# Optimization experiments

Measured on AMD Instinct MI355X. Metric: run time of the kernel, lower is better.

## Reference

```python
import jax, jax.numpy as jnp
import numpy as np

DIM_HEAD = 64
HEADS = 8

def rotate_half(x):
    x1, x2 = jnp.split(x, 2, axis=-1)
    return jnp.concatenate((-x2, x1), axis=-1)

def apply_rope(pos, t):
    # pos: [N, d] broadcast against t: [B, H, N, d]
    return t * jnp.cos(pos) + rotate_half(t) * jnp.sin(pos)

def setup_inputs() -> dict:
    key = jax.random.key(0)
    k1, k2, k3, k4 = jax.random.split(key, 4)
    B, N, C = 2, 4096, 512
    inner = HEADS * DIM_HEAD
    x = jax.random.normal(k1, (B, N, C), dtype=jnp.float32)
    pos_emb = jax.random.normal(k2, (N, DIM_HEAD), dtype=jnp.float32)
    w_qkv = jax.random.normal(k3, (C, inner * 3), dtype=jnp.float32) * (1.0 / np.sqrt(C))
    w_out = jax.random.normal(k4, (inner, C), dtype=jnp.float32) * (1.0 / np.sqrt(inner))
    b_out = jnp.zeros((C,), dtype=jnp.float32)
    return {"x": x, "pos_emb": pos_emb, "w_qkv": w_qkv, "w_out": w_out, "b_out": b_out}

def reference(x, pos_emb, w_qkv, w_out, b_out):
    B, N, C = x.shape
    scale = DIM_HEAD ** -0.5
    qkv = x @ w_qkv  # [B, N, 3*inner]
    q, k, v = jnp.split(qkv, 3, axis=-1)
    def to_heads(t):
        return t.reshape(B, N, HEADS, DIM_HEAD).transpose(0, 2, 1, 3)  # [B,H,N,d]
    q, k, v = to_heads(q), to_heads(k), to_heads(v)
    q = apply_rope(pos_emb, q)
    k = apply_rope(pos_emb, k)
    dots = jnp.einsum('bhid,bhjd->bhij', q, k) * scale  # [B,H,N,N]
    attn = jax.nn.softmax(dots, axis=-1)
    out = jnp.einsum('bhij,bhjd->bhid', attn, v)
    out = out.transpose(0, 2, 1, 3).reshape(B, N, HEADS * DIM_HEAD)
    return out @ w_out + b_out
```

## Files before the change

### kernel.cpp

```cpp
#include <hip/hip_runtime.h>


typedef float    floatx4 __attribute__((ext_vector_type(4)));
typedef _Float16 half8   __attribute__((ext_vector_type(8)));
typedef _Float16 half4   __attribute__((ext_vector_type(4)));

__device__ __forceinline__ float fast_exp2(float x) {
#if __has_builtin(__builtin_amdgcn_exp2f)
  return __builtin_amdgcn_exp2f(x);
#else
  float r;
  asm("v_exp_f32 %0, %1" : "=v"(r) : "v"(x));
  return r;
#endif
}

__device__ __forceinline__ void async16(const void* g, void* l) {
  __builtin_amdgcn_global_load_lds(
      (const __attribute__((address_space(1))) void*)g,
      (__attribute__((address_space(3))) void*)l, 16, 0, 0);
}

__global__ __launch_bounds__(256) void prep(
    const float* __restrict__ X, const float* __restrict__ pos,
    const float* __restrict__ Wqkv, const float* __restrict__ Wout,
    _Float16* __restrict__ A2, float2* __restrict__ CSSN,
    _Float16* __restrict__ B2qkv, _Float16* __restrict__ B2out) {
  __shared__ float tile[64][65];
  const int bid = blockIdx.x, t = threadIdx.x;
  if (bid < 4096) {
    const int i = (bid * 256 + t) * 4;
    const float4 v = *(const float4*)(X + i);
    half4 h;
    h[0] = (_Float16)v.x; h[1] = (_Float16)v.y;
    h[2] = (_Float16)v.z; h[3] = (_Float16)v.w;
    *(half4*)(A2 + i) = h;
  } else if (bid < 5120) {
    const int i = (bid - 4096) * 256 + t;
    const float p = pos[i];
    CSSN[i] = make_float2(__cosf(p), __sinf(p));
  } else {
    const float* W; _Float16* B2T; int Ncols, bx, by;
    if (bid < 5312) { const int idx = bid - 5120; bx = idx % 24; by = idx / 24;
                      W = Wqkv; B2T = B2qkv; Ncols = 1536; }
    else            { const int idx = bid - 5312; bx = idx % 8;  by = idx / 8;
                      W = Wout; B2T = B2out; Ncols = 512; }
    const int k0 = by * 64, n0 = bx * 64;
    const int lane = t & 63, w = t >> 6;
#pragma unroll 4
    for (int i = 0; i < 16; ++i) {
      const int k = w * 16 + i;
      tile[k][lane] = W[(size_t)(k0 + k) * Ncols + n0 + lane];
    }
    __syncthreads();
#pragma unroll 4
    for (int i = 0; i < 16; ++i) {
      const int n = w * 16 + i;
      B2T[(size_t)(n0 + n) * 512 + k0 + lane] = (_Float16)tile[lane][n];
    }
  }
}

__global__ __launch_bounds__(256) void gemm_qkv_rope(
    const _Float16* __restrict__ A2, const _Float16* __restrict__ B2T,
    const float2* __restrict__ CSSN,
    _Float16* __restrict__ Qb, _Float16* __restrict__ Kb,
    _Float16* __restrict__ VT) {
  __shared__ __align__(16) _Float16 ldsA[128 * 64];
  __shared__ __align__(16) _Float16 ldsB[128 * 64];
  const int t = threadIdx.x, w = t >> 6, l = t & 63;
  const int lo = l & 15, hi = l >> 4, sw = lo & 7;
  const int m0 = blockIdx.y << 7, n0 = blockIdx.x << 7;

  const int strow = w * 8 + (l >> 3);
  const int schunk = (l & 7) ^ ((l >> 3) & 7);
  const _Float16* gA = A2 + (size_t)(m0 + strow) * 512 + schunk * 8;
  const _Float16* gB = B2T + (size_t)(n0 + strow) * 512 + schunk * 8;
  _Float16* lA = ldsA + w * 512 + l * 8;
  _Float16* lB = ldsB + w * 512 + l * 8;

  const int mw = (w >> 1) * 64, nw = (w & 1) * 64;

  floatx4 acc[4][4];
#pragma unroll
  for (int mt = 0; mt < 4; ++mt)
#pragma unroll
    for (int nt = 0; nt < 4; ++nt) acc[mt][nt] = (floatx4){0.f, 0.f, 0.f, 0.f};

  for (int ks = 0; ks < 8; ++ks) {
    const int kk = ks * 64;
    __syncthreads();
#pragma unroll
    for (int i = 0; i < 4; ++i) {
      async16(gA + (size_t)i * 32 * 512 + kk, lA + i * 2048);
      async16(gB + (size_t)i * 32 * 512 + kk, lB + i * 2048);
    }
    __syncthreads();
#pragma unroll
    for (int kc = 0; kc < 2; ++kc) {
      const int slot = ((hi + 4 * kc) ^ sw) * 8;
      half8 af[4], bf[4];
#pragma unroll
      for (int mt = 0; mt < 4; ++mt)
        af[mt] = *(const half8*)(ldsA + (mw + mt * 16 + lo) * 64 + slot);
#pragma unroll
      for (int nt = 0; nt < 4; ++nt)
        bf[nt] = *(const half8*)(ldsB + (nw + nt * 16 + lo) * 64 + slot);
#pragma unroll
      for (int mt = 0; mt < 4; ++mt)
#pragma unroll
        for (int nt = 0; nt < 4; ++nt)
          acc[mt][nt] = __builtin_amdgcn_mfma_f32_16x16x32_f16(
              af[mt], bf[nt], acc[mt][nt], 0, 0, 0);
    }
  }

  const int bx = blockIdx.x;
  const int kind = bx >> 2;
  const int h = ((bx & 3) << 1) | (nw >> 6);
  if (kind == 2) {
#pragma unroll
    for (int mt = 0; mt < 4; ++mt) {
      const int rowb = m0 + mw + mt * 16 + hi * 4;
      const int b = rowb >> 12, nn = rowb & 4095;
#pragma unroll
      for (int nt = 0; nt < 4; ++nt) {
        const int dd = nt * 16 + lo;
        half4 v4;
#pragma unroll
        for (int r = 0; r < 4; ++r) v4[r] = (_Float16)acc[mt][nt][r];
        *(half4*)(VT + ((size_t)((b * 8 + h) * 64 + dd)) * 4096 + nn) = v4;
      }
    }
  } else {
    _Float16* Db = (kind == 0) ? Qb : Kb;
    const float sc = (kind == 0) ? 0.125f * 1.44269504f : 1.0f;
#pragma unroll
    for (int mt = 0; mt < 4; ++mt)
#pragma unroll
      for (int r = 0; r < 4; ++r) {
        const int row = m0 + mw + mt * 16 + hi * 4 + r;
        const int b = row >> 12, nn = row & 4095;
        const float2* cp = CSSN + (size_t)nn * 64 + lo;
        _Float16* orow = Db + ((size_t)((b * 8 + h) * 4096 + nn)) * 64 + lo;
#pragma unroll
        for (int nt = 0; nt < 4; ++nt) {
          const float2 cs = cp[nt * 16];
          const float x0 = acc[mt][nt][r];
          const float xp = acc[mt][nt ^ 2][r];
          const float rot = (nt & 2) ? xp : -xp;
          orow[nt * 16] = (_Float16)((x0 * cs.x + rot * cs.y) * sc);
        }
      }
  }
}

__global__ __launch_bounds__(256) void gemm_out_f16(
    const _Float16* __restrict__ A2, const _Float16* __restrict__ B2T,
    const float* __restrict__ bias, float* __restrict__ C) {
  __shared__ __align__(16) _Float16 ldsA[128 * 64];
  __shared__ __align__(16) _Float16 ldsB[64 * 64];
  const int t = threadIdx.x, w = t >> 6, l = t & 63;
  const int lo = l & 15, hi = l >> 4, sw = lo & 7;
  const int m0 = blockIdx.y << 7, n0 = blockIdx.x << 6;

  const int strow = w * 8 + (l >> 3);
  const int schunk = (l & 7) ^ ((l >> 3) & 7);
  const _Float16* gA = A2 + (size_t)(m0 + strow) * 512 + schunk * 8;
  const _Float16* gB = B2T + (size_t)(n0 + strow) * 512 + schunk * 8;
  _Float16* lA = ldsA + w * 512 + l * 8;
  _Float16* lB = ldsB + w * 512 + l * 8;

  const int mw = (w >> 1) * 64, nw = (w & 1) * 32;

  floatx4 acc[4][2];
#pragma unroll
  for (int mt = 0; mt < 4; ++mt)
#pragma unroll
    for (int nt = 0; nt < 2; ++nt) acc[mt][nt] = (floatx4){0.f, 0.f, 0.f, 0.f};

  for (int ks = 0; ks < 8; ++ks) {
    const int kk = ks * 64;
    __syncthreads();
#pragma unroll
    for (int i = 0; i < 4; ++i)
      async16(gA + (size_t)i * 32 * 512 + kk, lA + i * 2048);
#pragma unroll
    for (int i = 0; i < 2; ++i)
      async16(gB + (size_t)i * 32 * 512 + kk, lB + i * 2048);
    __syncthreads();
#pragma unroll
    for (int kc = 0; kc < 2; ++kc) {
      const int slot = ((hi + 4 * kc) ^ sw) * 8;
      half8 af[4], bf[2];
#pragma unroll
      for (int mt = 0; mt < 4; ++mt)
        af[mt] = *(const half8*)(ldsA + (mw + mt * 16 + lo) * 64 + slot);
#pragma unroll
      for (int nt = 0; nt < 2; ++nt)
        bf[nt] = *(const half8*)(ldsB + (nw + nt * 16 + lo) * 64 + slot);
#pragma unroll
      for (int mt = 0; mt < 4; ++mt)
#pragma unroll
        for (int nt = 0; nt < 2; ++nt)
          acc[mt][nt] = __builtin_amdgcn_mfma_f32_16x16x32_f16(
              af[mt], bf[nt], acc[mt][nt], 0, 0, 0);
    }
  }
#pragma unroll
  for (int mt = 0; mt < 4; ++mt)
#pragma unroll
    for (int r = 0; r < 4; ++r) {
      const int row = m0 + mw + mt * 16 + hi * 4 + r;
#pragma unroll
      for (int nt = 0; nt < 2; ++nt) {
        const int col = n0 + nw + nt * 16 + lo;
        C[(size_t)row * 512 + col] = acc[mt][nt][r] + bias[col];
      }
    }
}

__global__ __launch_bounds__(256, 4) void flash_attn(
    const _Float16* __restrict__ Qb, const _Float16* __restrict__ Kb,
    const _Float16* __restrict__ VT, _Float16* __restrict__ Opart,
    float* __restrict__ lpart) {
  __shared__ __align__(16) _Float16 ldsK[64 * 64];
  __shared__ __align__(16) _Float16 ldsV[64 * 64];
  const int t = threadIdx.x;
  const int w = t >> 6, l = t & 63;
  const int lo = l & 15, hi = l >> 4;
  const int sw = lo & 7;
  const int bh = blockIdx.y, qt = blockIdx.x, sp = blockIdx.z;

  const int srow = l >> 3;
  const int scol = (l & 7) ^ srow;
  const int goffK = srow * 64 + scol * 8;
  const size_t goffV = (size_t)srow * 4096 + scol * 8;
  const int ldst = l * 8;

  const _Float16* Qrow = Qb + ((size_t)bh * 4096 + qt * 128 + w * 32 + lo) * 64;
  half8 qf[2][2];
  qf[0][0] = *(const half8*)(Qrow + hi * 8);
  qf[0][1] = *(const half8*)(Qrow + hi * 8 + 32);
  qf[1][0] = *(const half8*)(Qrow + 16 * 64 + hi * 8);
  qf[1][1] = *(const half8*)(Qrow + 16 * 64 + hi * 8 + 32);

  const half4 onesf = (lo == 0) ? (half4){1.f16, 1.f16, 1.f16, 1.f16}
                                : (half4){0.f16, 0.f16, 0.f16, 0.f16};

  floatx4 acc[2][4];
  floatx4 l_acc[2];
#pragma unroll
  for (int g = 0; g < 2; ++g) {
    l_acc[g] = (floatx4){0.f, 0.f, 0.f, 0.f};
#pragma unroll
    for (int dt = 0; dt < 4; ++dt) acc[g][dt] = (floatx4){0.f, 0.f, 0.f, 0.f};
  }

  const _Float16* Kt = Kb + (size_t)bh * 4096 * 64;
  const _Float16* Vt = VT + (size_t)bh * 64 * 4096;

  for (int tt = sp * 32; tt < sp * 32 + 32; ++tt) {
    __syncthreads();
    {
      const _Float16* gK = Kt + (size_t)tt * 4096;
      const _Float16* gV = Vt + tt * 64;
      const int k0 = w * 2;
      async16(gK + (size_t)k0 * 512 + goffK,       ldsK + k0 * 512 + ldst);
      async16(gK + (size_t)(k0 + 1) * 512 + goffK, ldsK + (k0 + 1) * 512 + ldst);
      async16(gV + (size_t)k0 * 32768 + goffV,       ldsV + k0 * 512 + ldst);
      async16(gV + (size_t)(k0 + 1) * 32768 + goffV, ldsV + (k0 + 1) * 512 + ldst);
    }
    __syncthreads();

    floatx4 st[2][4];
#pragma unroll
    for (int jt = 0; jt < 4; ++jt) {
      const _Float16* kr = ldsK + (jt * 16 + lo) * 64;
      const half8 kf0 = *(const half8*)(kr + ((hi ^ sw) * 8));
      const half8 kf1 = *(const half8*)(kr + (((hi + 4) ^ sw) * 8));
#pragma unroll
      for (int g = 0; g < 2; ++g) {
        floatx4 z = (floatx4){0.f, 0.f, 0.f, 0.f};
        z = __builtin_amdgcn_mfma_f32_16x16x32_f16(kf0, qf[g][0], z, 0, 0, 0);
        z = __builtin_amdgcn_mfma_f32_16x16x32_f16(kf1, qf[g][1], z, 0, 0, 0);
        st[g][jt] = z;
      }
    }

    half4 pf[2][4];
#pragma unroll
    for (int g = 0; g < 2; ++g)
#pragma unroll
      for (int jt = 0; jt < 4; ++jt) {
        const float e0 = fast_exp2(st[g][jt][0]);
        const float e1 = fast_exp2(st[g][jt][1]);
        const float e2 = fast_exp2(st[g][jt][2]);
        const float e3 = fast_exp2(st[g][jt][3]);
        uint2 u;
        u.x = __builtin_bit_cast(unsigned, __builtin_amdgcn_cvt_pkrtz(e0, e1));
        u.y = __builtin_bit_cast(unsigned, __builtin_amdgcn_cvt_pkrtz(e2, e3));
        const half4 p4 = __builtin_bit_cast(half4, u);
        pf[g][jt] = p4;
        l_acc[g] = __builtin_amdgcn_mfma_f32_16x16x16f16(
            p4, onesf, l_acc[g], 0, 0, 0);
      }

#pragma unroll
    for (int dt = 0; dt < 4; ++dt) {
      half4 vf[4];
#pragma unroll
      for (int jt = 0; jt < 4; ++jt)
        vf[jt] = *(const half4*)(ldsV + (dt * 16 + lo) * 64 +
                                 (((jt * 2 + (hi >> 1)) ^ sw) * 8) + (hi & 1) * 4);
#pragma unroll
      for (int g = 0; g < 2; ++g)
#pragma unroll
        for (int jt = 0; jt < 4; ++jt)
          acc[g][dt] = __builtin_amdgcn_mfma_f32_16x16x16f16(
              pf[g][jt], vf[jt], acc[g][dt], 0, 0, 0);
    }
  }

  _Float16* obase = Opart + ((size_t)(sp * 16 + bh)) * 4096 * 64;
  float*    lbase = lpart + ((size_t)(sp * 16 + bh)) * 4096;
#pragma unroll
  for (int g = 0; g < 2; ++g)
#pragma unroll
    for (int r = 0; r < 4; ++r) {
      const int q = qt * 128 + w * 32 + g * 16 + hi * 4 + r;
      if (lo == 0) lbase[q] = l_acc[g][r];
#pragma unroll
      for (int dt = 0; dt < 4; ++dt)
        obase[(size_t)q * 64 + dt * 16 + lo] = (_Float16)acc[g][dt][r];
    }
}

__global__ __launch_bounds__(256) void combine_splits(
    const _Float16* __restrict__ Opart, const float* __restrict__ lpart,
    _Float16* __restrict__ O2) {
  const int idx = blockIdx.x * 256 + threadIdx.x;
  const int d0 = (idx & 15) * 4;
  const int q  = (idx >> 4) & 4095;
  const int bh = idx >> 16;
  const int b = bh >> 3, h = bh & 7;
  const half4 a0 = *(const half4*)(Opart + ((size_t)bh * 4096 + q) * 64 + d0);
  const half4 a1 = *(const half4*)(Opart + ((size_t)(16 + bh) * 4096 + q) * 64 + d0);
  const float lsum = lpart[(size_t)bh * 4096 + q] +
                     lpart[(size_t)(16 + bh) * 4096 + q];
  const float inv = 1.f / lsum;
  half4 o;
#pragma unroll
  for (int i = 0; i < 4; ++i)
    o[i] = (_Float16)(((float)a0[i] + (float)a1[i]) * inv);
  *(half4*)(O2 + ((size_t)(b * 4096 + q)) * 512 + h * 64 + d0) = o;
}

extern "C" void kernel_launch(void* const* d_in, const int* in_sizes, int n_in,
                              void* d_out, int out_size, void* d_ws, size_t ws_size,
                              hipStream_t stream) {
  const float* x     = (const float*)d_in[0];
  const float* pos   = (const float*)d_in[1];
  const float* w_qkv = (const float*)d_in[2];
  const float* w_out = (const float*)d_in[3];
  const float* b_out = (const float*)d_in[4];
  float* out = (float*)d_out;

  char* ws = (char*)d_ws;
  if (ws_size < (size_t)56 * 1024 * 1024) return;

  const size_t MB = 1024 * 1024;
  _Float16* A2x   = (_Float16*)ws;
  _Float16* O2    = (_Float16*)ws;
  _Float16* B2qkv = (_Float16*)(ws + 8 * MB);
  float2*   CSSN  = (float2*)(ws + 11 * MB);
  _Float16* Qb    = (_Float16*)(ws + 13 * MB);
  _Float16* Kb    = (_Float16*)(ws + 21 * MB);
  _Float16* VT    = (_Float16*)(ws + 29 * MB);
  _Float16* Opart = (_Float16*)(ws + 37 * MB);
  float*    lpart = (float*)(ws + 53 * MB);
  _Float16* B2out = (_Float16*)(ws + 54 * MB);

  prep<<<5376, 256, 0, stream>>>(x, pos, w_qkv, w_out, A2x, CSSN, B2qkv, B2out);
  gemm_qkv_rope<<<dim3(12, 64), 256, 0, stream>>>(A2x, B2qkv, CSSN, Qb, Kb, VT);
  flash_attn<<<dim3(32, 16, 2), 256, 0, stream>>>(Qb, Kb, VT, Opart, lpart);
  combine_splits<<<4096, 256, 0, stream>>>(Opart, lpart, O2);
  gemm_out_f16<<<dim3(8, 64), 256, 0, stream>>>(O2, B2out, b_out, out);
}
```

Baseline: 211.0 us.

## Stage RoPE Q/K output through LDS and replace row-sum MFMA with VALU shuffles

The QKV GEMM epilogue now writes rotated Q/K values into a per-wave padded LDS tile, then stores whole 16-byte rows to global memory, replacing scattered 2-byte stores. In attention, the softmax denominator is no longer accumulated with an extra MFMA against a ones vector. It is summed per lane in fp32 and reduced across lane groups with xor shuffles at the end. This removes 8 MFMAs per tile iteration and improves store coalescing, at the cost of extra LDS traffic and VALU adds; the row sum now uses unrounded fp32 exponentials rather than the fp16-rounded ones.

```diff
diff --git a/kernel.cpp b/kernel.cpp
--- a/kernel.cpp
+++ b/kernel.cpp
@@ -68,6 +68,7 @@
     _Float16* __restrict__ VT) {
   __shared__ __align__(16) _Float16 ldsA[128 * 64];
   __shared__ __align__(16) _Float16 ldsB[128 * 64];
+  __shared__ __align__(16) _Float16 qk_lds[4][16][72];
   const int t = threadIdx.x, w = t >> 6, l = t & 63;
   const int lo = l & 15, hi = l >> 4, sw = lo & 7;
   const int m0 = blockIdx.y << 7, n0 = blockIdx.x << 7;
@@ -135,23 +136,33 @@
   } else {
     _Float16* Db = (kind == 0) ? Qb : Kb;
     const float sc = (kind == 0) ? 0.125f * 1.44269504f : 1.0f;
-#pragma unroll
-    for (int mt = 0; mt < 4; ++mt)
+    _Float16 (*qt_)[72] = qk_lds[w];
+#pragma unroll
+    for (int mt = 0; mt < 4; ++mt) {
 #pragma unroll
       for (int r = 0; r < 4; ++r) {
         const int row = m0 + mw + mt * 16 + hi * 4 + r;
-        const int b = row >> 12, nn = row & 4095;
+        const int nn = row & 4095;
         const float2* cp = CSSN + (size_t)nn * 64 + lo;
-        _Float16* orow = Db + ((size_t)((b * 8 + h) * 4096 + nn)) * 64 + lo;
 #pragma unroll
         for (int nt = 0; nt < 4; ++nt) {
           const float2 cs = cp[nt * 16];
           const float x0 = acc[mt][nt][r];
           const float xp = acc[mt][nt ^ 2][r];
           const float rot = (nt & 2) ? xp : -xp;
-          orow[nt * 16] = (_Float16)((x0 * cs.x + rot * cs.y) * sc);
+          qt_[hi * 4 + r][nt * 16 + lo] = (_Float16)((x0 * cs.x + rot * cs.y) * sc);
         }
       }
+#pragma unroll
+      for (int pass = 0; pass < 2; ++pass) {
+        const int rr = pass * 8 + (l >> 3);
+        const int dcol = (l & 7) * 8;
+        const half8 v = *(const half8*)&qt_[rr][dcol];
+        const int row = m0 + mw + mt * 16 + rr;
+        const int b = row >> 12, nn = row & 4095;
+        *(half8*)(Db + ((size_t)((b * 8 + h) * 4096 + nn)) * 64 + dcol) = v;
+      }
+    }
   }
 }
 
@@ -245,17 +256,12 @@
   qf[1][0] = *(const half8*)(Qrow + 16 * 64 + hi * 8);
   qf[1][1] = *(const half8*)(Qrow + 16 * 64 + hi * 8 + 32);
 
-  const half4 onesf = (lo == 0) ? (half4){1.f16, 1.f16, 1.f16, 1.f16}
-                                : (half4){0.f16, 0.f16, 0.f16, 0.f16};
-
   floatx4 acc[2][4];
-  floatx4 l_acc[2];
-#pragma unroll
-  for (int g = 0; g < 2; ++g) {
-    l_acc[g] = (floatx4){0.f, 0.f, 0.f, 0.f};
+  float l_s[2] = {0.f, 0.f};
+#pragma unroll
+  for (int g = 0; g < 2; ++g)
 #pragma unroll
     for (int dt = 0; dt < 4; ++dt) acc[g][dt] = (floatx4){0.f, 0.f, 0.f, 0.f};
-  }
 
   const _Float16* Kt = Kb + (size_t)bh * 4096 * 64;
   const _Float16* Vt = VT + (size_t)bh * 64 * 4096;
@@ -297,13 +303,11 @@
         const float e1 = fast_exp2(st[g][jt][1]);
         const float e2 = fast_exp2(st[g][jt][2]);
         const float e3 = fast_exp2(st[g][jt][3]);
+        l_s[g] += (e0 + e1) + (e2 + e3);
         uint2 u;
         u.x = __builtin_bit_cast(unsigned, __builtin_amdgcn_cvt_pkrtz(e0, e1));
         u.y = __builtin_bit_cast(unsigned, __builtin_amdgcn_cvt_pkrtz(e2, e3));
-        const half4 p4 = __builtin_bit_cast(half4, u);
-        pf[g][jt] = p4;
-        l_acc[g] = __builtin_amdgcn_mfma_f32_16x16x16f16(
-            p4, onesf, l_acc[g], 0, 0, 0);
+        pf[g][jt] = __builtin_bit_cast(half4, u);
       }
 
 #pragma unroll
@@ -325,15 +329,20 @@
   _Float16* obase = Opart + ((size_t)(sp * 16 + bh)) * 4096 * 64;
   float*    lbase = lpart + ((size_t)(sp * 16 + bh)) * 4096;
 #pragma unroll
-  for (int g = 0; g < 2; ++g)
+  for (int g = 0; g < 2; ++g) {
+    float v = l_s[g];
+    v += __shfl_xor(v, 16);
+    v += __shfl_xor(v, 32);
+    if (hi == 0)
+      lbase[qt * 128 + w * 32 + g * 16 + lo] = v;
 #pragma unroll
     for (int r = 0; r < 4; ++r) {
       const int q = qt * 128 + w * 32 + g * 16 + hi * 4 + r;
-      if (lo == 0) lbase[q] = l_acc[g][r];
 #pragma unroll
       for (int dt = 0; dt < 4; ++dt)
         obase[(size_t)q * 64 + dt * 16 + lo] = (_Float16)acc[g][dt][r];
     }
+  }
 }
 
 __global__ __launch_bounds__(256) void combine_splits(
```

After: 206.3 us. 2.2% less time.
